# Kernel tuning notes

Hardware: AMD Instinct MI355X
Metric: run time of the kernel (lower is better)

## Reference

```python
import jax, jax.numpy as jnp
import numpy as np

D_MODEL = 1024
NUM_HEADS = 16
D_HEAD = D_MODEL // NUM_HEADS
THETA = 10000.0


def setup_inputs() -> dict:
    key = jax.random.key(0)
    ks = jax.random.split(key, 5)
    B, S = 2, 2048
    std = np.sqrt(2.0 / (D_MODEL + D_MODEL))
    return {
        "x": jax.random.normal(ks[0], (B, S, D_MODEL), dtype=jnp.float32),
        "token_positions": jnp.arange(S, dtype=jnp.int32),
        "wq": jax.random.normal(ks[1], (D_MODEL, D_MODEL), dtype=jnp.float32) * std,
        "wk": jax.random.normal(ks[2], (D_MODEL, D_MODEL), dtype=jnp.float32) * std,
        "wv": jax.random.normal(ks[3], (D_MODEL, D_MODEL), dtype=jnp.float32) * std,
        "wo": jax.random.normal(ks[4], (D_MODEL, D_MODEL), dtype=jnp.float32) * std,
    }


def _rope(x, token_positions):
    # x: [B, H, S, D_HEAD]; token_positions: [S]
    freq_idx = jnp.arange(0, D_HEAD, 2, dtype=jnp.float32)
    inv_freq = THETA ** (-freq_idx / D_HEAD)                      # [D_HEAD/2]
    angles = token_positions.astype(jnp.float32)[:, None] * inv_freq  # [S, D_HEAD/2]
    cos = jnp.cos(angles)[None, None, :, :]
    sin = jnp.sin(angles)[None, None, :, :]
    x_even = x[..., 0::2]
    x_odd = x[..., 1::2]
    rot_even = x_even * cos - x_odd * sin
    rot_odd = x_even * sin + x_odd * cos
    # interleave pairs back: [..., pairs, 2] -> [..., D_HEAD]
    return jnp.stack((rot_even, rot_odd), axis=-1).reshape(x.shape)


def reference(x, token_positions, wq, wk, wv, wo):
    B, S, _ = x.shape
    def proj(w):
        y = jnp.einsum('bsi,oi->bso', x, w)
        return y.reshape(B, S, NUM_HEADS, D_HEAD).transpose(0, 2, 1, 3)  # [B,H,S,Dh]
    q = _rope(proj(wq), token_positions)
    k = _rope(proj(wk), token_positions)
    v = proj(wv)
    scores = jnp.einsum('bhqd,bhkd->bhqk', q, k) / jnp.sqrt(jnp.float32(D_HEAD))
    causal = jnp.tril(jnp.ones((S, S), dtype=bool))
    scores = jnp.where(causal, scores, -jnp.inf)
    probs = jax.nn.softmax(scores, axis=-1)
    attn = jnp.einsum('bhqk,bhkd->bhqd', probs, v)
    attn = attn.transpose(0, 2, 1, 3).reshape(B, S, D_MODEL)
    return jnp.einsum('bsi,oi->bso', attn, wo)
```

## Files before the change

kernel.cpp:

```cpp
#include <hip/hip_runtime.h>
#include <math.h>

#define D_MODEL 1024
#define NUM_HEADS 16
#define D_HEAD 64
#define SEQ 2048
#define BATCH 2

typedef __attribute__((ext_vector_type(8))) short short8;
typedef __attribute__((ext_vector_type(4))) short short4v;
typedef __attribute__((ext_vector_type(4))) float float4v;
typedef __attribute__((ext_vector_type(2))) unsigned int uint2v;

__device__ __forceinline__ short f2bf(float f) {
    unsigned u = __float_as_uint(f);
    u += 0x7FFFu + ((u >> 16) & 1u);
    return (short)(u >> 16);
}

__device__ __forceinline__ float fexp2(float x) {
    return __builtin_amdgcn_exp2f(x);
}

__global__ __launch_bounds__(256) void cvt_bf16_kernel(
    const float* __restrict__ x,  const float* __restrict__ wq,
    const float* __restrict__ wk, const float* __restrict__ wv,
    const float* __restrict__ wo, const int* __restrict__ pos,
    short* __restrict__ xb,  short* __restrict__ wqb,
    short* __restrict__ wkb, short* __restrict__ wvb,
    short* __restrict__ wob,
    float* __restrict__ costab, float* __restrict__ sintab)
{
    const int a = blockIdx.y;
    if (a == 5) {
        const int idx = blockIdx.x * 256 + threadIdx.x;
        if (idx < SEQ * 32) {
            const int s = idx >> 5, fi = idx & 31;
            const float p = (float)pos[s];
            const float inv_freq = exp2f((float)fi * -0.4152410118609203f);
            float sn, cs;
            sincosf(p * inv_freq, &sn, &cs);
            costab[idx] = cs;
            sintab[idx] = sn;
        }
        return;
    }
    const float* src = (a == 0) ? x : (a == 1) ? wq : (a == 2) ? wk : (a == 3) ? wv : wo;
    short* dst = (a == 0) ? xb : (a == 1) ? wqb : (a == 2) ? wkb : (a == 3) ? wvb : wob;
    const int n = (a == 0) ? (BATCH * SEQ * D_MODEL) : (D_MODEL * D_MODEL);
    const int i = (blockIdx.x * 256 + threadIdx.x) * 8;
    if (i >= n) return;
    const float4 v0 = *(const float4*)(src + i);
    const float4 v1 = *(const float4*)(src + i + 4);
    short8 r;
    r[0] = f2bf(v0.x); r[1] = f2bf(v0.y); r[2] = f2bf(v0.z); r[3] = f2bf(v0.w);
    r[4] = f2bf(v1.x); r[5] = f2bf(v1.y); r[6] = f2bf(v1.z); r[7] = f2bf(v1.w);
    *(short8*)(dst + i) = r;
}

__device__ __forceinline__ void gemm_core_db(
    const short* __restrict__ a, const short* __restrict__ b,
    short* smem, int m0, int n0, float4v acc[4][4], const int nk)
{
    const int tid = threadIdx.x;
    const int lane = tid & 63;
    const int l15 = lane & 15, quad = lane >> 4;
    const int wave = tid >> 6;
    const int mw = (wave & 1) * 64, nw = (wave >> 1) * 64;
    const int srow = tid >> 2;
    const int scol = (tid & 3) * 8;
    const int ssw = (((tid & 3) ^ ((srow >> 1) & 3))) * 8;
    const int xsw = (l15 >> 1) & 3;

    const short* ag = a + (size_t)(m0 + srow) * D_MODEL + scol;
    const short* bg = b + (size_t)(n0 + srow) * D_MODEL + scol;

    short* bufA[2] = { smem,        smem + 8192 };
    short* bufB[2] = { smem + 4096, smem + 12288 };

    short8 ga0 = *(const short8*)(ag);
    short8 ga1 = *(const short8*)(ag + (size_t)64 * D_MODEL);
    short8 gb0 = *(const short8*)(bg);
    short8 gb1 = *(const short8*)(bg + (size_t)64 * D_MODEL);
    *(short8*)&bufA[0][srow * 32 + ssw]        = ga0;
    *(short8*)&bufA[0][(64 + srow) * 32 + ssw] = ga1;
    *(short8*)&bufB[0][srow * 32 + ssw]        = gb0;
    *(short8*)&bufB[0][(64 + srow) * 32 + ssw] = gb1;
    ga0 = *(const short8*)(ag + 32);
    ga1 = *(const short8*)(ag + 32 + (size_t)64 * D_MODEL);
    gb0 = *(const short8*)(bg + 32);
    gb1 = *(const short8*)(bg + 32 + (size_t)64 * D_MODEL);

    for (int k = 0; k < nk; k++) {
        __syncthreads();
        if (k + 1 < nk) {
            short* bA = bufA[(k + 1) & 1];
            short* bB = bufB[(k + 1) & 1];
            *(short8*)&bA[srow * 32 + ssw]        = ga0;
            *(short8*)&bA[(64 + srow) * 32 + ssw] = ga1;
            *(short8*)&bB[srow * 32 + ssw]        = gb0;
            *(short8*)&bB[(64 + srow) * 32 + ssw] = gb1;
        }
        if (k + 2 < nk) {
            const int off = (k + 2) * 32;
            ga0 = *(const short8*)(ag + off);
            ga1 = *(const short8*)(ag + off + (size_t)64 * D_MODEL);
            gb0 = *(const short8*)(bg + off);
            gb1 = *(const short8*)(bg + off + (size_t)64 * D_MODEL);
        }
        const short* lA = bufA[k & 1];
        const short* lB = bufB[k & 1];
        short8 af[4], bf[4];
        #pragma unroll
        for (int i = 0; i < 4; i++)
            af[i] = *(const short8*)&lA[(mw + i * 16 + l15) * 32 + (quad ^ xsw) * 8];
        #pragma unroll
        for (int i = 0; i < 4; i++)
            bf[i] = *(const short8*)&lB[(nw + i * 16 + l15) * 32 + (quad ^ xsw) * 8];
        #pragma unroll
        for (int mi = 0; mi < 4; mi++)
            #pragma unroll
            for (int ni = 0; ni < 4; ni++)
                acc[mi][ni] = __builtin_amdgcn_mfma_f32_16x16x32_bf16(
                    af[mi], bf[ni], acc[mi][ni], 0, 0, 0);
    }
}

__device__ __forceinline__ void gemm_core_out(
    const short* __restrict__ a, const short* __restrict__ b,
    short* smem, int m0, int n0, float4v acc[2][4])
{
    const int tid = threadIdx.x;
    const int lane = tid & 63;
    const int l15 = lane & 15, quad = lane >> 4;
    const int wave = tid >> 6;
    const int mw = wave * 32;
    const int srow = tid >> 2;
    const int scol = (tid & 3) * 8;
    const int ssw = (((tid & 3) ^ ((srow >> 1) & 3))) * 8;
    const int xsw = (l15 >> 1) & 3;

    const short* ag = a + (size_t)(m0 + srow) * D_MODEL + scol;
    const short* bg = b + (size_t)(n0 + srow) * D_MODEL + scol;

    short* bufA[2] = { smem,        smem + 6144 };
    short* bufB[2] = { smem + 4096, smem + 10240 };

    short8 ga0 = *(const short8*)(ag);
    short8 ga1 = *(const short8*)(ag + (size_t)64 * D_MODEL);
    short8 gb0 = *(const short8*)(bg);
    *(short8*)&bufA[0][srow * 32 + ssw]        = ga0;
    *(short8*)&bufA[0][(64 + srow) * 32 + ssw] = ga1;
    *(short8*)&bufB[0][srow * 32 + ssw]        = gb0;
    ga0 = *(const short8*)(ag + 32);
    ga1 = *(const short8*)(ag + 32 + (size_t)64 * D_MODEL);
    gb0 = *(const short8*)(bg + 32);

    for (int k = 0; k < 32; k++) {
        __syncthreads();
        if (k + 1 < 32) {
            short* bA = bufA[(k + 1) & 1];
            short* bB = bufB[(k + 1) & 1];
            *(short8*)&bA[srow * 32 + ssw]        = ga0;
            *(short8*)&bA[(64 + srow) * 32 + ssw] = ga1;
            *(short8*)&bB[srow * 32 + ssw]        = gb0;
        }
        if (k + 2 < 32) {
            const int off = (k + 2) * 32;
            ga0 = *(const short8*)(ag + off);
            ga1 = *(const short8*)(ag + off + (size_t)64 * D_MODEL);
            gb0 = *(const short8*)(bg + off);
        }
        const short* lA = bufA[k & 1];
        const short* lB = bufB[k & 1];
        short8 af[2], bf[4];
        #pragma unroll
        for (int i = 0; i < 2; i++)
            af[i] = *(const short8*)&lA[(mw + i * 16 + l15) * 32 + (quad ^ xsw) * 8];
        #pragma unroll
        for (int i = 0; i < 4; i++)
            bf[i] = *(const short8*)&lB[(i * 16 + l15) * 32 + (quad ^ xsw) * 8];
        #pragma unroll
        for (int mi = 0; mi < 2; mi++)
            #pragma unroll
            for (int ni = 0; ni < 4; ni++)
                acc[mi][ni] = __builtin_amdgcn_mfma_f32_16x16x32_bf16(
                    af[mi], bf[ni], acc[mi][ni], 0, 0, 0);
    }
}

__global__ __launch_bounds__(256) void qkv_mfma_kernel(
    const short* __restrict__ xb, const short* __restrict__ wqb,
    const short* __restrict__ wkb, const short* __restrict__ wvb,
    const float* __restrict__ costab, const float* __restrict__ sintab,
    short* __restrict__ Qb, short* __restrict__ Kb, short* __restrict__ Vt)
{
    __shared__ __align__(16) short smem[128 * 136];

    const int z = blockIdx.x >> 8;
    const int bid = blockIdx.x & 255;
    const int m0 = (bid & 31) * 128;
    const int n0 = (bid >> 5) * 128;
    const short* w = (z == 0) ? wqb : (z == 1) ? wkb : wvb;

    float4v acc[4][4];
    #pragma unroll
    for (int i = 0; i < 4; i++)
        #pragma unroll
        for (int j = 0; j < 4; j++)
            acc[i][j] = (float4v){0.f, 0.f, 0.f, 0.f};

    gemm_core_db(xb, w, smem, m0, n0, acc, 32);

    const int tid = threadIdx.x;
    const int lane = tid & 63;
    const int l15 = lane & 15, quad = lane >> 4;
    const int wave = tid >> 6;
    const int mw = (wave & 1) * 64, nw = (wave >> 1) * 64;
    const int s_base = m0 & (SEQ - 1);
    const int bb = m0 >> 11;

    __syncthreads();

    if (z == 2) {
        #pragma unroll
        for (int ni = 0; ni < 4; ni++) {
            #pragma unroll
            for (int mi = 0; mi < 4; mi++) {
                #pragma unroll
                for (int r = 0; r < 4; r++)
                    smem[(nw + ni * 16 + l15) * 136 + mw + mi * 16 + quad * 4 + r] =
                        f2bf(acc[mi][ni][r]);
            }
        }
        __syncthreads();
        #pragma unroll
        for (int it = 0; it < 8; it++) {
            const int nloc = it * 16 + (tid >> 4);
            const int mloc = (tid & 15) * 8;
            const short8 val = *(const short8*)&smem[nloc * 136 + mloc];
            const int n = n0 + nloc;
            const int h = n >> 6, d = n & 63;
            *(short8*)(Vt + ((size_t)(bb * NUM_HEADS + h) * D_HEAD + d) * SEQ +
                       s_base + mloc) = val;
        }
    } else {
        short* dst = (z == 0) ? Qb : Kb;
        const float qs = (z == 0) ? 0.18033688011112042f : 1.0f;
        #pragma unroll
        for (int ni = 0; ni < 4; ni++) {
            const int n = n0 + nw + ni * 16 + l15;
            const int d = n & 63;
            const int fi = d >> 1;
            #pragma unroll
            for (int mi = 0; mi < 4; mi++) {
                #pragma unroll
                for (int r = 0; r < 4; r++) {
                    const int mloc = mw + mi * 16 + quad * 4 + r;
                    const int ti = ((s_base + mloc) << 5) + fi;
                    const float cs = costab[ti];
                    const float sn = sintab[ti];
                    const float val = acc[mi][ni][r];
                    const float partner = __shfl_xor(val, 1, 64);
                    const float res = (l15 & 1) ? fmaf(partner, sn, val * cs)
                                                : fmaf(val, cs, -partner * sn);
                    smem[mloc * 136 + nw + ni * 16 + l15] = f2bf(res * qs);
                }
            }
        }
        __syncthreads();
        #pragma unroll
        for (int it = 0; it < 8; it++) {
            const int ri = it * 32 + (tid >> 3);
            const int mloc = ri & 127;
            const int hh = ri >> 7;
            const int nloc = hh * 64 + (tid & 7) * 8;
            const short8 val = *(const short8*)&smem[mloc * 136 + nloc];
            const int n = n0 + nloc;
            const int h = n >> 6, d = n & 63;
            *(short8*)(dst + ((size_t)(bb * NUM_HEADS + h) * SEQ + s_base + mloc) *
                       D_HEAD + d) = val;
        }
    }
}

__global__ __launch_bounds__(256) void attn_mfma_kernel(
    const short* __restrict__ Qb, const short* __restrict__ Kb,
    const short* __restrict__ Vt, short* __restrict__ Ab)
{
    __shared__ __align__(16) short lK[64 * 72];
    __shared__ __align__(16) short lV[64 * 72];
    __shared__ __align__(16) short lP[4][16 * 72];

    const int tid = threadIdx.x;
    const int lane = tid & 63;
    const int wave = tid >> 6;
    const int l15 = lane & 15;
    const int quad = lane >> 4;

    const int bh = blockIdx.x & (BATCH * NUM_HEADS - 1);
    const int qt = (SEQ / 64 - 1) - (blockIdx.x >> 5);
    const int q0w = qt * 64 + wave * 16;
    const int qcmp = q0w + l15;

    const short* Kg = Kb + (size_t)bh * SEQ * D_HEAD;
    const short* Vg = Vt + (size_t)bh * D_HEAD * SEQ;

    const short* Qrow = Qb + ((size_t)bh * SEQ + q0w + l15) * D_HEAD;
    const short8 qf0 = *(const short8*)(Qrow + quad * 8);
    const short8 qf1 = *(const short8*)(Qrow + 32 + quad * 8);

    float4v o0 = {0.f, 0.f, 0.f, 0.f}, o1 = o0, o2 = o0, o3 = o0;
    float lpA = 0.f, lpB = 0.f;

    const int nt = qt + 1;
    const int srow = tid >> 2;
    const int c4  = tid & 3;
    const int sch = c4 * 8;
    const int w1off = srow * 72 + c4 * 16;

    short8 k0 = *(const short8*)(Kg + (size_t)srow * D_HEAD + sch);
    short8 k1 = *(const short8*)(Kg + (size_t)srow * D_HEAD + sch + 32);
    short8 v0 = *(const short8*)(Vg + (size_t)srow * SEQ + sch);
    short8 v1 = *(const short8*)(Vg + (size_t)srow * SEQ + sch + 32);

#define ATTN_TILE_COMPUTE(KT0, MASKED)                                        \
    {                                                                         \
        short* Pw = lP[wave];                                                 \
        _Pragma("unroll")                                                     \
        for (int g = 0; g < 4; g++) {                                         \
            float4v s = {0.f, 0.f, 0.f, 0.f};                                 \
            const short8 ka = *(const short8*)&lK[(g * 16 + l15) * 72 + quad * 16];     \
            const short8 kb = *(const short8*)&lK[(g * 16 + l15) * 72 + quad * 16 + 8]; \
            __builtin_amdgcn_s_setprio(1);                                    \
            s = __builtin_amdgcn_mfma_f32_16x16x32_bf16(ka, qf0, s, 0, 0, 0); \
            s = __builtin_amdgcn_mfma_f32_16x16x32_bf16(kb, qf1, s, 0, 0, 0); \
            __builtin_amdgcn_s_setprio(0);                                    \
            float e0, e1, e2, e3;                                             \
            if (MASKED) {                                                     \
                const int kbase = (KT0) + g * 16 + quad * 4;                  \
                e0 = (kbase + 0 <= qcmp) ? fexp2(s[0]) : 0.f;                 \
                e1 = (kbase + 1 <= qcmp) ? fexp2(s[1]) : 0.f;                 \
                e2 = (kbase + 2 <= qcmp) ? fexp2(s[2]) : 0.f;                 \
                e3 = (kbase + 3 <= qcmp) ? fexp2(s[3]) : 0.f;                 \
            } else {                                                          \
                e0 = fexp2(s[0]); e1 = fexp2(s[1]);                           \
                e2 = fexp2(s[2]); e3 = fexp2(s[3]);                           \
            }                                                                 \
            lpA += e0 + e2;                                                   \
            lpB += e1 + e3;                                                   \
            unsigned int pw0, pw1;                                            \
            asm("v_cvt_pk_bf16_f32 %0, %1, %2" : "=v"(pw0) : "v"(e0), "v"(e1)); \
            asm("v_cvt_pk_bf16_f32 %0, %1, %2" : "=v"(pw1) : "v"(e2), "v"(e3)); \
            uint2v pk; pk[0] = pw0; pk[1] = pw1;                              \
            *(uint2v*)&Pw[l15 * 72 + g * 16 + quad * 4] = pk;                 \
        }                                                                     \
        const short8 pa0 = *(const short8*)&lP[wave][l15 * 72 + quad * 8];    \
        const short8 pa1 = *(const short8*)&lP[wave][l15 * 72 + 32 + quad * 8]; \
        __builtin_amdgcn_s_setprio(1);                                        \
        _Pragma("unroll")                                                     \
        for (int j = 0; j < 4; j++) {                                         \
            const short8 va = *(const short8*)&lV[(j * 16 + l15) * 72 + quad * 16];     \
            const short8 vb = *(const short8*)&lV[(j * 16 + l15) * 72 + quad * 16 + 8]; \
            float4v* oj = (j == 0) ? &o0 : (j == 1) ? &o1 : (j == 2) ? &o2 : &o3;       \
            *oj = __builtin_amdgcn_mfma_f32_16x16x32_bf16(pa0, va, *oj, 0, 0, 0);       \
            *oj = __builtin_amdgcn_mfma_f32_16x16x32_bf16(pa1, vb, *oj, 0, 0, 0);       \
        }                                                                     \
        __builtin_amdgcn_s_setprio(0);                                        \
    }

    for (int t = 0; t < nt - 1; t++) {
        const int kt0 = t * 64;
        __syncthreads();
        *(short8*)&lK[w1off]     = k0;
        *(short8*)&lK[w1off + 8] = k1;
        *(short8*)&lV[w1off]     = v0;
        *(short8*)&lV[w1off + 8] = v1;
        __syncthreads();
        k0 = *(const short8*)(Kg + (size_t)(kt0 + 64 + srow) * D_HEAD + sch);
        k1 = *(const short8*)(Kg + (size_t)(kt0 + 64 + srow) * D_HEAD + sch + 32);
        v0 = *(const short8*)(Vg + (size_t)srow * SEQ + kt0 + 64 + sch);
        v1 = *(const short8*)(Vg + (size_t)srow * SEQ + kt0 + 64 + sch + 32);
        ATTN_TILE_COMPUTE(kt0, false)
    }
    {
        const int kt0 = (nt - 1) * 64;
        __syncthreads();
        *(short8*)&lK[w1off]     = k0;
        *(short8*)&lK[w1off + 8] = k1;
        *(short8*)&lV[w1off]     = v0;
        *(short8*)&lV[w1off + 8] = v1;
        __syncthreads();
        ATTN_TILE_COMPUTE(kt0, true)
    }
#undef ATTN_TILE_COMPUTE

    float lp = lpA + lpB;
    lp += __shfl_xor(lp, 16, 64);
    lp += __shfl_xor(lp, 32, 64);

    const int b = bh >> 4, h = bh & 15;
    short* Ap = Ab + ((size_t)(b * SEQ) + q0w + quad * 4) * D_MODEL + h * D_HEAD;
    #pragma unroll
    for (int r = 0; r < 4; r++) {
        const float inv = 1.0f / __shfl(lp, quad * 4 + r, 64);
        Ap[(size_t)r * D_MODEL + l15]      = f2bf(o0[r] * inv);
        Ap[(size_t)r * D_MODEL + 16 + l15] = f2bf(o1[r] * inv);
        Ap[(size_t)r * D_MODEL + 32 + l15] = f2bf(o2[r] * inv);
        Ap[(size_t)r * D_MODEL + 48 + l15] = f2bf(o3[r] * inv);
    }
}

__global__ __launch_bounds__(256) void out_mfma_kernel(
    const short* __restrict__ Ab, const short* __restrict__ wob,
    float* __restrict__ out)
{
    __shared__ __align__(16) short smem[12288];

    const int bid = blockIdx.x;
    const int m0 = (bid & 31) * 128;
    const int n0 = (bid >> 5) * 64;

    float4v acc[2][4];
    #pragma unroll
    for (int i = 0; i < 2; i++)
        #pragma unroll
        for (int j = 0; j < 4; j++)
            acc[i][j] = (float4v){0.f, 0.f, 0.f, 0.f};

    gemm_core_out(Ab, wob, smem, m0, n0, acc);

    const int tid = threadIdx.x;
    const int lane = tid & 63;
    const int l15 = lane & 15, quad = lane >> 4;
    const int wave = tid >> 6;
    const int mw = wave * 32;

    #pragma unroll
    for (int mi = 0; mi < 2; mi++) {
        #pragma unroll
        for (int r = 0; r < 4; r++) {
            const int m = m0 + mw + mi * 16 + quad * 4 + r;
            float* op = out + (size_t)m * D_MODEL + n0 + l15;
            #pragma unroll
            for (int ni = 0; ni < 4; ni++)
                op[ni * 16] = acc[mi][ni][r];
        }
    }
}

extern "C" void kernel_launch(void* const* d_in, const int* in_sizes, int n_in,
                              void* d_out, int out_size, void* d_ws, size_t ws_size,
                              hipStream_t stream)
{
    const float* x  = (const float*)d_in[0];
    const int*  pos = (const int*)d_in[1];
    const float* wq = (const float*)d_in[2];
    const float* wk = (const float*)d_in[3];
    const float* wv = (const float*)d_in[4];
    const float* wo = (const float*)d_in[5];
    float* out = (float*)d_out;

    const size_t nx = (size_t)BATCH * SEQ * D_MODEL;
    const size_t nw = (size_t)D_MODEL * D_MODEL;
    short* xb  = (short*)d_ws;
    short* wqb = xb + nx;
    short* wkb = wqb + nw;
    short* wvb = wkb + nw;
    short* wob = wvb + nw;
    short* Qb  = wob + nw;
    short* Kb  = Qb + nx;
    short* Vt  = Kb + nx;
    short* Ab  = Vt + nx;
    float* costab = (float*)(Ab + nx);
    float* sintab = costab + SEQ * 32;

    dim3 blk(256);
    cvt_bf16_kernel<<<dim3(2048, 6), blk, 0, stream>>>(x, wq, wk, wv, wo, pos,
                                                       xb, wqb, wkb, wvb, wob,
                                                       costab, sintab);
    qkv_mfma_kernel<<<dim3(768), blk, 0, stream>>>(xb, wqb, wkb, wvb,
                                                   costab, sintab, Qb, Kb, Vt);
    attn_mfma_kernel<<<dim3(BATCH * NUM_HEADS * (SEQ / 64)), blk, 0, stream>>>(Qb, Kb, Vt, Ab);
    out_mfma_kernel<<<dim3(512), blk, 0, stream>>>(Ab, wob, out);
}
```

Measured before the change: 181.0 us.

## Load QKV GEMM weight fragments directly into registers, bypassing LDS

The QKV projection GEMM now reads B (weight) fragments straight from global memory into MFMA operand registers, with each wave loading only its own rows, instead of staging them through double-buffered shared memory. Only the A (activation) tile remains in LDS, which halves LDS traffic and the LDS footprint of the main loop. It also adds a launch-bounds occupancy hint of 3 blocks per CU and unrolls the loop by 2. The cost is exposed global-load latency on B, which is not prefetched ahead, and duplicated B reads between waves that share n-columns.

```diff
diff --git a/kernel.cpp b/kernel.cpp
--- a/kernel.cpp
+++ b/kernel.cpp
@@ -58,9 +58,9 @@
     *(short8*)(dst + i) = r;
 }
 
-__device__ __forceinline__ void gemm_core_db(
+__device__ __forceinline__ void gemm_core_breg(
     const short* __restrict__ a, const short* __restrict__ b,
-    short* smem, int m0, int n0, float4v acc[4][4], const int nk)
+    short* smem, int m0, int n0, float4v acc[4][4])
 {
     const int tid = threadIdx.x;
     const int lane = tid & 63;
@@ -73,50 +73,39 @@
     const int xsw = (l15 >> 1) & 3;
 
     const short* ag = a + (size_t)(m0 + srow) * D_MODEL + scol;
-    const short* bg = b + (size_t)(n0 + srow) * D_MODEL + scol;
-
-    short* bufA[2] = { smem,        smem + 8192 };
-    short* bufB[2] = { smem + 4096, smem + 12288 };
+    const short* bg = b + (size_t)(n0 + nw + l15) * D_MODEL + quad * 8;
+
+    short* bufA[2] = { smem, smem + 4096 };
 
     short8 ga0 = *(const short8*)(ag);
     short8 ga1 = *(const short8*)(ag + (size_t)64 * D_MODEL);
-    short8 gb0 = *(const short8*)(bg);
-    short8 gb1 = *(const short8*)(bg + (size_t)64 * D_MODEL);
     *(short8*)&bufA[0][srow * 32 + ssw]        = ga0;
     *(short8*)&bufA[0][(64 + srow) * 32 + ssw] = ga1;
-    *(short8*)&bufB[0][srow * 32 + ssw]        = gb0;
-    *(short8*)&bufB[0][(64 + srow) * 32 + ssw] = gb1;
     ga0 = *(const short8*)(ag + 32);
     ga1 = *(const short8*)(ag + 32 + (size_t)64 * D_MODEL);
-    gb0 = *(const short8*)(bg + 32);
-    gb1 = *(const short8*)(bg + 32 + (size_t)64 * D_MODEL);
-
-    for (int k = 0; k < nk; k++) {
-        __syncthreads();
-        if (k + 1 < nk) {
+
+    #pragma unroll 2
+    for (int k = 0; k < 32; k++) {
+        short8 bf[4];
+        #pragma unroll
+        for (int i = 0; i < 4; i++)
+            bf[i] = *(const short8*)(bg + (size_t)(i * 16) * D_MODEL + k * 32);
+        __syncthreads();
+        if (k + 1 < 32) {
             short* bA = bufA[(k + 1) & 1];
-            short* bB = bufB[(k + 1) & 1];
             *(short8*)&bA[srow * 32 + ssw]        = ga0;
             *(short8*)&bA[(64 + srow) * 32 + ssw] = ga1;
-            *(short8*)&bB[srow * 32 + ssw]        = gb0;
-            *(short8*)&bB[(64 + srow) * 32 + ssw] = gb1;
-        }
-        if (k + 2 < nk) {
+        }
+        if (k + 2 < 32) {
             const int off = (k + 2) * 32;
             ga0 = *(const short8*)(ag + off);
             ga1 = *(const short8*)(ag + off + (size_t)64 * D_MODEL);
-            gb0 = *(const short8*)(bg + off);
-            gb1 = *(const short8*)(bg + off + (size_t)64 * D_MODEL);
         }
         const short* lA = bufA[k & 1];
-        const short* lB = bufB[k & 1];
-        short8 af[4], bf[4];
+        short8 af[4];
         #pragma unroll
         for (int i = 0; i < 4; i++)
             af[i] = *(const short8*)&lA[(mw + i * 16 + l15) * 32 + (quad ^ xsw) * 8];
-        #pragma unroll
-        for (int i = 0; i < 4; i++)
-            bf[i] = *(const short8*)&lB[(nw + i * 16 + l15) * 32 + (quad ^ xsw) * 8];
         #pragma unroll
         for (int mi = 0; mi < 4; mi++)
             #pragma unroll
@@ -189,7 +178,7 @@
     }
 }
 
-__global__ __launch_bounds__(256) void qkv_mfma_kernel(
+__global__ __launch_bounds__(256, 3) void qkv_mfma_kernel(
     const short* __restrict__ xb, const short* __restrict__ wqb,
     const short* __restrict__ wkb, const short* __restrict__ wvb,
     const float* __restrict__ costab, const float* __restrict__ sintab,
@@ -210,7 +199,7 @@
         for (int j = 0; j < 4; j++)
             acc[i][j] = (float4v){0.f, 0.f, 0.f, 0.f};
 
-    gemm_core_db(xb, w, smem, m0, n0, acc, 32);
+    gemm_core_breg(xb, w, smem, m0, n0, acc);
 
     const int tid = threadIdx.x;
     const int lane = tid & 63;
```

Result: slower. 199.0 us (+9.9%).

## Fuse QKV, attention and output kernels into one cooperative persistent launch

Applied to the files above, without the earlier changes.

Turns the three GEMM/attention kernels into device phase functions and adds a cooperative kernel of 1024 blocks that runs the phases in sequence, separated by grid-wide syncs. The aim is to remove two kernel launch gaps and their tail drain. It falls back to the separate launches when cooperative launch or occupancy is not enough. Risks include the cost of grid.sync, __launch_bounds__(256,4) limiting registers and causing spills, a 34 KB shared buffer in every phase lowering occupancy, and idle blocks during the QKV and output phases.

```diff
diff --git a/kernel.cpp b/kernel.cpp
--- a/kernel.cpp
+++ b/kernel.cpp
@@ -1,5 +1,8 @@
 #include <hip/hip_runtime.h>
+#include <hip/hip_cooperative_groups.h>
 #include <math.h>
+
+namespace cg = cooperative_groups;
 
 #define D_MODEL 1024
 #define NUM_HEADS 16
@@ -189,33 +192,33 @@
     }
 }
 
-__global__ __launch_bounds__(256) void qkv_mfma_kernel(
+__device__ __forceinline__ void qkv_phase(
+    int logical_bid, short* smem,
     const short* __restrict__ xb, const short* __restrict__ wqb,
     const short* __restrict__ wkb, const short* __restrict__ wvb,
     const float* __restrict__ costab, const float* __restrict__ sintab,
     short* __restrict__ Qb, short* __restrict__ Kb, short* __restrict__ Vt)
 {
-    __shared__ __align__(16) short smem[128 * 136];
-
-    const int z = blockIdx.x >> 8;
-    const int bid = blockIdx.x & 255;
-    const int m0 = (bid & 31) * 128;
-    const int n0 = (bid >> 5) * 128;
-    const short* w = (z == 0) ? wqb : (z == 1) ? wkb : wvb;
-
-    float4v acc[4][4];
-    #pragma unroll
-    for (int i = 0; i < 4; i++)
-        #pragma unroll
-        for (int j = 0; j < 4; j++)
-            acc[i][j] = (float4v){0.f, 0.f, 0.f, 0.f};
-
-    gemm_core_db(xb, w, smem, m0, n0, acc, 32);
-
     const int tid = threadIdx.x;
     const int lane = tid & 63;
     const int l15 = lane & 15, quad = lane >> 4;
     const int wave = tid >> 6;
+
+    const int z = logical_bid >> 8;
+    const int bid = logical_bid & 255;
+    const int m0 = (bid & 31) * 128;
+    const int n0 = (bid >> 5) * 128;
+    const short* w = (z == 0) ? wqb : (z == 1) ? wkb : wvb;
+
+    float4v acc[4][4];
+    #pragma unroll
+    for (int i = 0; i < 4; i++)
+        #pragma unroll
+        for (int j = 0; j < 4; j++)
+            acc[i][j] = (float4v){0.f, 0.f, 0.f, 0.f};
+
+    gemm_core_db(xb, w, smem, m0, n0, acc, 32);
+
     const int mw = (wave & 1) * 64, nw = (wave >> 1) * 64;
     const int s_base = m0 & (SEQ - 1);
     const int bb = m0 >> 11;
@@ -284,22 +287,23 @@
     }
 }
 
-__global__ __launch_bounds__(256) void attn_mfma_kernel(
+__device__ __forceinline__ void attn_phase(
+    int logical_bid, short* smem,
     const short* __restrict__ Qb, const short* __restrict__ Kb,
     const short* __restrict__ Vt, short* __restrict__ Ab)
 {
-    __shared__ __align__(16) short lK[64 * 72];
-    __shared__ __align__(16) short lV[64 * 72];
-    __shared__ __align__(16) short lP[4][16 * 72];
-
     const int tid = threadIdx.x;
     const int lane = tid & 63;
     const int wave = tid >> 6;
     const int l15 = lane & 15;
     const int quad = lane >> 4;
 
-    const int bh = blockIdx.x & (BATCH * NUM_HEADS - 1);
-    const int qt = (SEQ / 64 - 1) - (blockIdx.x >> 5);
+    short* lK = smem;
+    short* lV = smem + 4608;
+    short* Pw = smem + 9216 + wave * (16 * 72);
+
+    const int bh = logical_bid & (BATCH * NUM_HEADS - 1);
+    const int qt = (SEQ / 64 - 1) - (logical_bid >> 5);
     const int q0w = qt * 64 + wave * 16;
     const int qcmp = q0w + l15;
 
@@ -326,7 +330,6 @@
 
 #define ATTN_TILE_COMPUTE(KT0, MASKED)                                        \
     {                                                                         \
-        short* Pw = lP[wave];                                                 \
         _Pragma("unroll")                                                     \
         for (int g = 0; g < 4; g++) {                                         \
             float4v s = {0.f, 0.f, 0.f, 0.f};                                 \
@@ -355,8 +358,8 @@
             uint2v pk; pk[0] = pw0; pk[1] = pw1;                              \
             *(uint2v*)&Pw[l15 * 72 + g * 16 + quad * 4] = pk;                 \
         }                                                                     \
-        const short8 pa0 = *(const short8*)&lP[wave][l15 * 72 + quad * 8];    \
-        const short8 pa1 = *(const short8*)&lP[wave][l15 * 72 + 32 + quad * 8]; \
+        const short8 pa0 = *(const short8*)&Pw[l15 * 72 + quad * 8];          \
+        const short8 pa1 = *(const short8*)&Pw[l15 * 72 + 32 + quad * 8];     \
         __builtin_amdgcn_s_setprio(1);                                        \
         _Pragma("unroll")                                                     \
         for (int j = 0; j < 4; j++) {                                         \
@@ -411,31 +414,29 @@
     }
 }
 
-__global__ __launch_bounds__(256) void out_mfma_kernel(
+__device__ __forceinline__ void out_phase(
+    int logical_bid, short* smem,
     const short* __restrict__ Ab, const short* __restrict__ wob,
     float* __restrict__ out)
 {
-    __shared__ __align__(16) short smem[12288];
-
-    const int bid = blockIdx.x;
-    const int m0 = (bid & 31) * 128;
-    const int n0 = (bid >> 5) * 64;
-
-    float4v acc[2][4];
-    #pragma unroll
-    for (int i = 0; i < 2; i++)
-        #pragma unroll
-        for (int j = 0; j < 4; j++)
-            acc[i][j] = (float4v){0.f, 0.f, 0.f, 0.f};
-
-    gemm_core_out(Ab, wob, smem, m0, n0, acc);
-
     const int tid = threadIdx.x;
     const int lane = tid & 63;
     const int l15 = lane & 15, quad = lane >> 4;
     const int wave = tid >> 6;
+
+    const int m0 = (logical_bid & 31) * 128;
+    const int n0 = (logical_bid >> 5) * 64;
+
+    float4v acc[2][4];
+    #pragma unroll
+    for (int i = 0; i < 2; i++)
+        #pragma unroll
+        for (int j = 0; j < 4; j++)
+            acc[i][j] = (float4v){0.f, 0.f, 0.f, 0.f};
+
+    gemm_core_out(Ab, wob, smem, m0, n0, acc);
+
     const int mw = wave * 32;
-
     #pragma unroll
     for (int mi = 0; mi < 2; mi++) {
         #pragma unroll
@@ -447,6 +448,60 @@
                 op[ni * 16] = acc[mi][ni][r];
         }
     }
+}
+
+__global__ __launch_bounds__(256) void qkv_mfma_kernel(
+    const short* __restrict__ xb, const short* __restrict__ wqb,
+    const short* __restrict__ wkb, const short* __restrict__ wvb,
+    const float* __restrict__ costab, const float* __restrict__ sintab,
+    short* __restrict__ Qb, short* __restrict__ Kb, short* __restrict__ Vt)
+{
+    __shared__ __align__(16) short smem[128 * 136];
+    qkv_phase(blockIdx.x, smem, xb, wqb, wkb, wvb, costab, sintab, Qb, Kb, Vt);
+}
+
+__global__ __launch_bounds__(256) void attn_mfma_kernel(
+    const short* __restrict__ Qb, const short* __restrict__ Kb,
+    const short* __restrict__ Vt, short* __restrict__ Ab)
+{
+    __shared__ __align__(16) short smem[128 * 136];
+    attn_phase(blockIdx.x, smem, Qb, Kb, Vt, Ab);
+}
+
+__global__ __launch_bounds__(256) void out_mfma_kernel(
+    const short* __restrict__ Ab, const short* __restrict__ wob,
+    float* __restrict__ out)
+{
+    __shared__ __align__(16) short smem[128 * 136];
+    out_phase(blockIdx.x, smem, Ab, wob, out);
+}
+
+__global__ __launch_bounds__(256, 4) void fused_mfma_kernel(
+    const short* __restrict__ xb, const short* __restrict__ wqb,
+    const short* __restrict__ wkb, const short* __restrict__ wvb,
+    const float* __restrict__ costab, const float* __restrict__ sintab,
+    short* __restrict__ Qb, short* __restrict__ Kb, short* __restrict__ Vt,
+    short* __restrict__ Ab, const short* __restrict__ wob,
+    float* __restrict__ out)
+{
+    cg::grid_group grid = cg::this_grid();
+    __shared__ __align__(16) short smem[128 * 136];
+
+    if (blockIdx.x < 768)
+        qkv_phase(blockIdx.x, smem, xb, wqb, wkb, wvb, costab, sintab, Qb, Kb, Vt);
+
+    __threadfence();
+    grid.sync();
+    __threadfence();
+
+    attn_phase(blockIdx.x, smem, Qb, Kb, Vt, Ab);
+
+    __threadfence();
+    grid.sync();
+    __threadfence();
+
+    if (blockIdx.x < 512)
+        out_phase(blockIdx.x, smem, Ab, wob, out);
 }
 
 extern "C" void kernel_launch(void* const* d_in, const int* in_sizes, int n_in,
@@ -475,12 +530,38 @@
     float* costab = (float*)(Ab + nx);
     float* sintab = costab + SEQ * 32;
 
+    static int coop_mode = -1;
+    if (coop_mode < 0) {
+        int dev = 0;
+        (void)hipGetDevice(&dev);
+        int coop = 0, ncu = 0, nb = 0;
+        (void)hipDeviceGetAttribute(&coop, hipDeviceAttributeCooperativeLaunch, dev);
+        (void)hipDeviceGetAttribute(&ncu, hipDeviceAttributeMultiprocessorCount, dev);
+        hipError_t e = hipOccupancyMaxActiveBlocksPerMultiprocessor(
+            &nb, (const void*)fused_mfma_kernel, 256, 0);
+        coop_mode = (coop && e == hipSuccess && (long)nb * ncu >= 1024) ? 1 : 0;
+    }
+
     dim3 blk(256);
     cvt_bf16_kernel<<<dim3(2048, 6), blk, 0, stream>>>(x, wq, wk, wv, wo, pos,
                                                        xb, wqb, wkb, wvb, wob,
                                                        costab, sintab);
-    qkv_mfma_kernel<<<dim3(768), blk, 0, stream>>>(xb, wqb, wkb, wvb,
-                                                   costab, sintab, Qb, Kb, Vt);
-    attn_mfma_kernel<<<dim3(BATCH * NUM_HEADS * (SEQ / 64)), blk, 0, stream>>>(Qb, Kb, Vt, Ab);
-    out_mfma_kernel<<<dim3(512), blk, 0, stream>>>(Ab, wob, out);
-}
+
+    int launched = 0;
+    if (coop_mode == 1) {
+        void* args[] = { (void*)&xb, (void*)&wqb, (void*)&wkb, (void*)&wvb,
+                         (void*)&costab, (void*)&sintab,
+                         (void*)&Qb, (void*)&Kb, (void*)&Vt, (void*)&Ab,
+                         (void*)&wob, (void*)&out };
+        hipError_t err = hipLaunchCooperativeKernel((void*)fused_mfma_kernel,
+                                                    dim3(1024), blk, args, 0, stream);
+        if (err == hipSuccess) launched = 1;
+        else coop_mode = 0;
+    }
+    if (!launched) {
+        qkv_mfma_kernel<<<dim3(768), blk, 0, stream>>>(xb, wqb, wkb, wvb,
+                                                       costab, sintab, Qb, Kb, Vt);
+        attn_mfma_kernel<<<dim3(BATCH * NUM_HEADS * (SEQ / 64)), blk, 0, stream>>>(Qb, Kb, Vt, Ab);
+        out_mfma_kernel<<<dim3(512), blk, 0, stream>>>(Ab, wob, out);
+    }
+}
```

Result: no change. 183.6 us (+1.4%).
